# Performance work log

Measured on AMD Instinct MI355X. Metric: run time of the kernel, lower is better.

Reference implementation:

```python
import jax, jax.numpy as jnp
import numpy as np

ENC_DIM = 64

def setup_inputs() -> dict:
    key = jax.random.key(0)
    ks = jax.random.split(key, 7)
    B, C, H, W = 16, 64, 128, 128
    s = 1.0 / np.sqrt(C)
    return {
        "x": jax.random.normal(ks[0], (B, C, H, W), jnp.float32),
        "wq_w": jax.random.normal(ks[1], (ENC_DIM, C), jnp.float32) * s,
        "wq_b": jax.random.normal(ks[2], (ENC_DIM,), jnp.float32) * 0.01,
        "wk_w": jax.random.normal(ks[3], (ENC_DIM, C), jnp.float32) * s,
        "wk_b": jax.random.normal(ks[4], (ENC_DIM,), jnp.float32) * 0.01,
        "wv_w": jax.random.normal(ks[5], (ENC_DIM, C), jnp.float32) * s,
        "wv_b": jax.random.normal(ks[6], (ENC_DIM,), jnp.float32) * 0.01,
    }

def _conv1x1(x, w, b):
    # 1x1 conv == per-pixel linear: [B,C,H,W] x [E,C] -> [B,E,H,W]
    return jnp.einsum('bchw,ec->behw', x, w) + b[None, :, None, None]

def reference(x, wq_w, wq_b, wk_w, wk_b, wv_w, wv_b):
    scaler = jnp.sqrt(jnp.asarray(ENC_DIM, x.dtype))
    Q = _conv1x1(x, wq_w, wq_b)  # [B,E,H,W]
    K = _conv1x1(x, wk_w, wk_b)
    V = _conv1x1(x, wv_w, wv_b)
    # scores = Q @ K^T over last two dims -> [B,E,H,H]
    scores = jnp.einsum('behw,bekw->behk', Q, K) / scaler
    temp1 = jax.nn.softmax(scores, axis=-1)          # softmax over last dim; dropout is identity (eval)
    # Q^T @ K -> [B,E,W,W], softmax over dim -2
    t2 = jnp.einsum('behw,behv->bewv', Q, K) / scaler
    temp2 = jax.nn.softmax(t2, axis=-2)
    # temp1 @ V @ temp2 -> [B,E,H,W]
    tv = jnp.einsum('behk,bekw->behw', temp1, V)
    return jnp.einsum('behw,bewv->behv', tv, temp2)
```

## Files before the change

### kernel.cpp

```cpp
#include <hip/hip_runtime.h>
#include <hip/hip_bf16.h>

typedef __attribute__((ext_vector_type(8))) short short8;
typedef __attribute__((ext_vector_type(4))) float f32x4;

#define MFMA16(a, b, c) __builtin_amdgcn_mfma_f32_16x16x32_bf16((a), (b), (c), 0, 0, 0)

__device__ __forceinline__ short f2bf(float f) {
  union { float f; unsigned u; } v; v.f = f;
  unsigned r = v.u + 0x7fffu + ((v.u >> 16) & 1u);
  return (short)(r >> 16);
}
__device__ __forceinline__ unsigned pack2(float lo, float hi) {
  return (unsigned)(unsigned short)f2bf(lo) | ((unsigned)(unsigned short)f2bf(hi) << 16);
}

__global__ __launch_bounds__(256) void qkv_kernel(
    const float* __restrict__ x,
    const float* __restrict__ wq, const float* __restrict__ bq,
    const float* __restrict__ wk, const float* __restrict__ bk,
    const float* __restrict__ wv, const float* __restrict__ bv,
    short* __restrict__ Q, short* __restrict__ K, short* __restrict__ V)
{
  __shared__ alignas(16) short xs[64 * 256];
  __shared__ alignas(16) short ws[3 * 64 * 64];
  __shared__ float bs[3 * 64];

  const int t    = threadIdx.x;
  const int b    = blockIdx.x >> 6;
  const int pt   = blockIdx.x & 63;
  const int pix0 = pt << 8;
  const float* xb = x + ((size_t)b << 20);

  #pragma unroll
  for (int i = 0; i < 16; ++i) {
    int f4 = i * 256 + t;
    int c  = f4 >> 6;
    int p4 = (f4 & 63) << 2;
    const float4 v = *reinterpret_cast<const float4*>(xb + c * 16384 + pix0 + p4);
    short* d = &xs[c * 256 + p4];
    d[0] = f2bf(v.x); d[1] = f2bf(v.y); d[2] = f2bf(v.z); d[3] = f2bf(v.w);
  }
  {
    #pragma unroll
    for (int i = 0; i < 16; ++i) {
      int idx = i * 256 + t;
      int e = idx >> 6, c = idx & 63;
      int d = e * 64 + (c ^ ((e & 7) << 3));
      ws[d]        = f2bf(wq[idx]);
      ws[d + 4096] = f2bf(wk[idx]);
      ws[d + 8192] = f2bf(wv[idx]);
    }
    if (t < 192) bs[t] = (t < 64) ? bq[t] : ((t < 128) ? bk[t - 64] : bv[t - 128]);
  }
  __syncthreads();

  const int lane = t & 63;
  const int wid  = t >> 6;
  const int p0   = wid << 6;
  const int l15  = lane & 15;
  const int lg   = lane >> 4;

  short8 bfrag[4][2];
  #pragma unroll
  for (int nt = 0; nt < 4; ++nt) {
    int pix = p0 + nt * 16 + l15;
    #pragma unroll
    for (int ks = 0; ks < 2; ++ks) {
      int cb = ks * 32 + (lg << 3);
      short8 f;
      #pragma unroll
      for (int j = 0; j < 8; ++j) f[j] = xs[(cb + j) * 256 + pix];
      bfrag[nt][ks] = f;
    }
  }

  #pragma unroll
  for (int m = 0; m < 3; ++m) {
    short* op = (m == 0) ? Q : ((m == 1) ? K : V);
    short8 afrag[4][2];
    #pragma unroll
    for (int mt = 0; mt < 4; ++mt) {
      int e = mt * 16 + l15;
      #pragma unroll
      for (int ks = 0; ks < 2; ++ks) {
        int cb8 = (ks * 4 + lg) ^ (e & 7);
        afrag[mt][ks] = *reinterpret_cast<const short8*>(&ws[m * 4096 + e * 64 + cb8 * 8]);
      }
    }
    #pragma unroll
    for (int mt = 0; mt < 4; ++mt) {
      #pragma unroll
      for (int nt = 0; nt < 4; ++nt) {
        f32x4 acc = {0.f, 0.f, 0.f, 0.f};
        acc = MFMA16(afrag[mt][0], bfrag[nt][0], acc);
        acc = MFMA16(afrag[mt][1], bfrag[nt][1], acc);
        int e_base = mt * 16 + (lg << 2);
        int pix = pix0 + p0 + nt * 16 + l15;
        #pragma unroll
        for (int r = 0; r < 4; ++r) {
          int e = e_base + r;
          float val = acc[r] + bs[m * 64 + e];
          op[(((size_t)b * 64 + e) << 14) + pix] = f2bf(val);
        }
      }
    }
  }
}

__global__ __launch_bounds__(256, 2) void attn_kernel(
    const short* __restrict__ Qg, const short* __restrict__ Kg,
    const short* __restrict__ Vg, float* __restrict__ out)
{
  __shared__ alignas(16) short B1[128 * 128];
  __shared__ alignas(16) short B2[128 * 128];

  const int t = threadIdx.x;
  const size_t base = (size_t)blockIdx.x << 14;

  auto stage = [&](short* dst, const short* src) {
    #pragma unroll
    for (int i = 0; i < 8; ++i) {
      int eb  = i * 256 + t;
      int row = eb >> 4;
      int cb  = eb & 15;
      float4 v = *reinterpret_cast<const float4*>(src + (eb << 3));
      *reinterpret_cast<float4*>(dst + row * 128 + ((cb ^ (row & 15)) << 3)) = v;
    }
  };

  const int w  = t & 127;
  const int rb = (t >> 7) << 6;

  auto colgather = [&](const short* src, unsigned* p) {
    #pragma unroll
    for (int k2 = 0; k2 < 32; ++k2) {
      int r0 = rb + 2 * k2;
      int r1 = r0 + 1;
      unsigned a  = (unsigned short)src[r0 * 128 + (w ^ ((r0 & 15) << 3))];
      unsigned b_ = (unsigned short)src[r1 * 128 + (w ^ ((r1 & 15) << 3))];
      p[k2] = a | (b_ << 16);
    }
  };
  auto t_write = [&](short* dst, const unsigned* p) {
    const int w15 = w & 15;
    #pragma unroll
    for (int k8 = 0; k8 < 8; ++k8) {
      int hb = (rb >> 3) + k8;
      *reinterpret_cast<short8*>(&dst[w * 128 + ((hb ^ w15) << 3)]) =
          *reinterpret_cast<const short8*>(&p[k8 * 4]);
    }
  };
  auto vload = [&](const short* Vsrc, unsigned* p) {
    #pragma unroll
    for (int k2 = 0; k2 < 32; ++k2) {
      unsigned a  = (unsigned short)Vsrc[(rb + 2 * k2) * 128 + w];
      unsigned b_ = (unsigned short)Vsrc[(rb + 2 * k2 + 1) * 128 + w];
      p[k2] = a | (b_ << 16);
    }
  };

  const int lane = t & 63;
  const int wid  = t >> 6;
  const int m0   = wid << 5;
  const int l15  = lane & 15;
  const int lg   = lane >> 4;

  f32x4 acc0[8], acc1[8];

  auto matmul = [&](const short* bufA, const short* bufB) {
    short8 af0[4], af1[4];
    const short* ba[4];
    #pragma unroll
    for (int ks = 0; ks < 4; ++ks) {
      const int xorb = ((ks * 4 + lg) ^ l15) << 3;
      af0[ks] = *reinterpret_cast<const short8*>(&bufA[(m0 + l15) * 128 + xorb]);
      af1[ks] = *reinterpret_cast<const short8*>(&bufA[(m0 + 16 + l15) * 128 + xorb]);
      ba[ks] = &bufB[l15 * 128 + xorb];
    }
    #pragma unroll
    for (int n = 0; n < 8; ++n) {
      f32x4 a0 = {0.f, 0.f, 0.f, 0.f};
      f32x4 a1 = {0.f, 0.f, 0.f, 0.f};
      #pragma unroll
      for (int ks = 0; ks < 4; ++ks) {
        short8 bf = *reinterpret_cast<const short8*>(ba[ks] + n * 2048);
        a0 = MFMA16(af0[ks], bf, a0);
        a1 = MFMA16(af1[ks], bf, a1);
      }
      acc0[n] = a0; acc1[n] = a1;
    }
  };

  auto softmax_pack = [&](f32x4* acc, unsigned* pk) {
    #pragma unroll
    for (int r = 0; r < 4; ++r) {
      float mx = acc[0][r];
      #pragma unroll
      for (int n = 1; n < 8; ++n) mx = fmaxf(mx, acc[n][r]);
      mx = fmaxf(mx, __shfl_xor(mx, 1));
      mx = fmaxf(mx, __shfl_xor(mx, 2));
      mx = fmaxf(mx, __shfl_xor(mx, 4));
      mx = fmaxf(mx, __shfl_xor(mx, 8));
      float p[8]; float s = 0.f;
      #pragma unroll
      for (int n = 0; n < 8; ++n) { p[n] = __expf((acc[n][r] - mx) * 0.125f); s += p[n]; }
      s += __shfl_xor(s, 1); s += __shfl_xor(s, 2);
      s += __shfl_xor(s, 4); s += __shfl_xor(s, 8);
      float inv = 1.0f / s;
      #pragma unroll
      for (int np = 0; np < 4; ++np)
        pk[r * 4 + np] = pack2(p[2 * np] * inv, p[2 * np + 1] * inv);
    }
  };

  auto store_pk = [&](short* dst, const unsigned* pk, int mbase) {
    #pragma unroll
    for (int r = 0; r < 4; ++r) {
      int row = mbase + (lg << 2) + r;
      int sw  = (row & 15) << 3;
      short* dr = dst + row * 128;
      #pragma unroll
      for (int np = 0; np < 4; ++np) {
        unsigned v = pk[r * 4 + np];
        int c0 = (2 * np) * 16 + l15;
        dr[c0 ^ sw]        = (short)(v & 0xffff);
        dr[(c0 + 16) ^ sw] = (short)(v >> 16);
      }
    }
  };
  auto store_accs = [&](short* dst) {
    unsigned tv[16];
    #pragma unroll
    for (int r = 0; r < 4; ++r)
      #pragma unroll
      for (int np = 0; np < 4; ++np)
        tv[r * 4 + np] = pack2(acc0[2 * np][r], acc0[2 * np + 1][r]);
    store_pk(dst, tv, m0);
    #pragma unroll
    for (int r = 0; r < 4; ++r)
      #pragma unroll
      for (int np = 0; np < 4; ++np)
        tv[r * 4 + np] = pack2(acc1[2 * np][r], acc1[2 * np + 1][r]);
    store_pk(dst, tv, m0 + 16);
  };

  unsigned t1[32], t2[32];

  stage(B1, Qg + base);
  stage(B2, Kg + base);
  __syncthreads();

  matmul(B1, B2);
  softmax_pack(acc0, t1);
  softmax_pack(acc1, t1 + 16);
  unsigned qc[32], kc[32];
  colgather(B1, qc);
  colgather(B2, kc);
  __syncthreads();

  t_write(B1, qc);
  t_write(B2, kc);
  __syncthreads();

  matmul(B2, B1);
  softmax_pack(acc0, t2);
  softmax_pack(acc1, t2 + 16);
  __syncthreads();

  {
    unsigned vc[32];
    vload(Vg + base, vc);
    store_pk(B1, t1, m0);
    store_pk(B1, t1 + 16, m0 + 16);
    t_write(B2, vc);
  }
  __syncthreads();

  matmul(B1, B2);
  store_accs(B1);
  __syncthreads();

  store_pk(B2, t2, m0);
  store_pk(B2, t2 + 16, m0 + 16);
  __syncthreads();

  {
    float* ob = out + base;
    short8 af0[4], af1[4];
    const short* ba[4];
    #pragma unroll
    for (int ks = 0; ks < 4; ++ks) {
      const int xorb = ((ks * 4 + lg) ^ l15) << 3;
      af0[ks] = *reinterpret_cast<const short8*>(&B1[(m0 + l15) * 128 + xorb]);
      af1[ks] = *reinterpret_cast<const short8*>(&B1[(m0 + 16 + l15) * 128 + xorb]);
      ba[ks] = &B2[l15 * 128 + xorb];
    }
    #pragma unroll
    for (int n = 0; n < 8; ++n) {
      f32x4 a0 = {0.f, 0.f, 0.f, 0.f};
      f32x4 a1 = {0.f, 0.f, 0.f, 0.f};
      #pragma unroll
      for (int ks = 0; ks < 4; ++ks) {
        short8 bf = *reinterpret_cast<const short8*>(ba[ks] + n * 2048);
        a0 = MFMA16(af0[ks], bf, a0);
        a1 = MFMA16(af1[ks], bf, a1);
      }
      #pragma unroll
      for (int r = 0; r < 4; ++r) {
        int row0 = m0 + (lg << 2) + r;
        ob[row0 * 128 + n * 16 + l15] = a0[r];
        ob[(row0 + 16) * 128 + n * 16 + l15] = a1[r];
      }
    }
  }
}

extern "C" void kernel_launch(void* const* d_in, const int* in_sizes, int n_in,
                              void* d_out, int out_size, void* d_ws, size_t ws_size,
                              hipStream_t stream) {
  const float* x  = (const float*)d_in[0];
  const float* wq = (const float*)d_in[1];
  const float* bq = (const float*)d_in[2];
  const float* wk = (const float*)d_in[3];
  const float* bk = (const float*)d_in[4];
  const float* wv = (const float*)d_in[5];
  const float* bv = (const float*)d_in[6];

  const size_t N = (size_t)16 * 64 * 128 * 128;
  short* Q = (short*)d_ws;
  short* K = Q + N;
  short* V = K + N;

  qkv_kernel<<<1024, 256, 0, stream>>>(x, wq, bq, wk, bk, wv, bv, Q, K, V);
  attn_kernel<<<1024, 256, 0, stream>>>(Q, K, V, (float*)d_out);
}
```

Baseline: 86.75 us.

## Use four LDS buffers to cut barriers and prefetch V early in attention kernel

The attention kernel now allocates four 32KB LDS buffers instead of two, so transposed Q/K go to separate buffers. This removes several __syncthreads barriers, and the V global load is issued before the first matmul so it overlaps compute. The cost is 128KB of LDS per block with launch bounds lowered to one block per CU, which halves occupancy. More registers are also held live (vc across the matmuls).

```diff
diff --git a/kernel.cpp b/kernel.cpp
--- a/kernel.cpp
+++ b/kernel.cpp
@@ -108,12 +108,15 @@
   }
 }
 
-__global__ __launch_bounds__(256, 2) void attn_kernel(
+__global__ __launch_bounds__(256, 1) void attn_kernel(
     const short* __restrict__ Qg, const short* __restrict__ Kg,
     const short* __restrict__ Vg, float* __restrict__ out)
 {
-  __shared__ alignas(16) short B1[128 * 128];
-  __shared__ alignas(16) short B2[128 * 128];
+  __shared__ alignas(16) short lds[4 * 16384];
+  short* B1 = lds;
+  short* B2 = lds + 16384;
+  short* B3 = lds + 2 * 16384;
+  short* B4 = lds + 3 * 16384;
 
   const int t = threadIdx.x;
   const size_t base = (size_t)blockIdx.x << 14;
@@ -245,44 +248,40 @@
     store_pk(dst, tv, m0 + 16);
   };
 
-  unsigned t1[32], t2[32];
+  unsigned t1[32], t2[32], vc[32];
 
   stage(B1, Qg + base);
   stage(B2, Kg + base);
   __syncthreads();
 
+  vload(Vg + base, vc);
   matmul(B1, B2);
   softmax_pack(acc0, t1);
   softmax_pack(acc1, t1 + 16);
-  unsigned qc[32], kc[32];
-  colgather(B1, qc);
-  colgather(B2, kc);
-  __syncthreads();
-
-  t_write(B1, qc);
-  t_write(B2, kc);
-  __syncthreads();
-
-  matmul(B2, B1);
+  {
+    unsigned qc[32];
+    colgather(B1, qc);
+    t_write(B3, qc);
+  }
+  {
+    unsigned kc[32];
+    colgather(B2, kc);
+    t_write(B4, kc);
+  }
+  __syncthreads();
+
+  store_pk(B1, t1, m0);
+  store_pk(B1, t1 + 16, m0 + 16);
+  t_write(B2, vc);
+  matmul(B4, B3);
   softmax_pack(acc0, t2);
   softmax_pack(acc1, t2 + 16);
   __syncthreads();
 
-  {
-    unsigned vc[32];
-    vload(Vg + base, vc);
-    store_pk(B1, t1, m0);
-    store_pk(B1, t1 + 16, m0 + 16);
-    t_write(B2, vc);
-  }
-  __syncthreads();
-
   matmul(B1, B2);
   store_accs(B1);
-  __syncthreads();
-
-  store_pk(B2, t2, m0);
-  store_pk(B2, t2 + 16, m0 + 16);
+  store_pk(B4, t2, m0);
+  store_pk(B4, t2 + 16, m0 + 16);
   __syncthreads();
 
   {
@@ -294,7 +293,7 @@
       const int xorb = ((ks * 4 + lg) ^ l15) << 3;
       af0[ks] = *reinterpret_cast<const short8*>(&B1[(m0 + l15) * 128 + xorb]);
       af1[ks] = *reinterpret_cast<const short8*>(&B1[(m0 + 16 + l15) * 128 + xorb]);
-      ba[ks] = &B2[l15 * 128 + xorb];
+      ba[ks] = &B4[l15 * 128 + xorb];
     }
     #pragma unroll
     for (int n = 0; n < 8; ++n) {
```

Result: slower. 153.9 us (+77.4%).
